# Kernel tuning notes

Measured on AMD Instinct MI355X. Metric: run time of the kernel, lower is better.

## Reference

```python
import jax, jax.numpy as jnp
import numpy as np

EMBED = 8      # == n_qubits, forced by x[:, i, :].view(batch, n_qubits)
FFN = 4096
B, S = 32, 2048


def setup_inputs() -> dict:
    key = jax.random.key(0)
    k_x, k_t, k_w1, k_b1, k_w2, k_b2 = jax.random.split(key, 6)
    x = jax.random.normal(k_x, (B, S, EMBED), dtype=jnp.float32)
    theta = jax.random.normal(k_t, (), dtype=jnp.float32)  # shared trainable RY angle
    # torch.nn.Linear-style init bounds
    lim1 = 1.0 / np.sqrt(EMBED)
    lim2 = 1.0 / np.sqrt(FFN)
    W1 = jax.random.uniform(k_w1, (FFN, EMBED), jnp.float32, -lim1, lim1)
    b1 = jax.random.uniform(k_b1, (FFN,), jnp.float32, -lim1, lim1)
    W2 = jax.random.uniform(k_w2, (EMBED, FFN), jnp.float32, -lim2, lim2)
    b2 = jax.random.uniform(k_b2, (EMBED,), jnp.float32, -lim2, lim2)
    return {"x": x, "theta": theta, "W1": W1, "b1": b1, "W2": W2, "b2": b2}


def reference(x, theta, W1, b1, W2, b2):
    # Quantum circuit, solved analytically (product state, single-qubit gates):
    # |0> --RX(x_i)--RY(theta)--> <Z_i> = cos(theta) * cos(x_i)
    # This fuses the original per-token Python loop into one elementwise op.
    q = jnp.cos(theta) * jnp.cos(x)                 # [B, S, 8]
    # dropout is identity in eval mode
    h = jax.nn.relu(jnp.einsum('bsk,fk->bsf', q, W1) + b1)   # [B, S, FFN]
    out = jnp.einsum('bsf,ef->bse', h, W2) + b2              # [B, S, 8]
    return out
```

## Files before the change

kernel.cpp:

```cpp
#include <hip/hip_runtime.h>
#include <math.h>

#define FFN_DIM 4096
#define NCHUNK  128

typedef _Float16 f16x8 __attribute__((ext_vector_type(8)));
typedef __fp16   h16x2 __attribute__((ext_vector_type(2)));
typedef float    f32x16 __attribute__((ext_vector_type(16)));
typedef float    f32x4  __attribute__((ext_vector_type(4)));

__global__ void build_frags_kernel(const float* __restrict__ w1,
                                   const float* __restrict__ b1,
                                   const float* __restrict__ w2,
                                   _Float16* __restrict__ w1f,
                                   _Float16* __restrict__ w2f) {
    int i = blockIdx.x * 256 + threadIdx.x;
    if (i < NCHUNK * 64 * 8) {
        int j    = i & 7;
        int lane = (i >> 3) & 63;
        int cc   = i >> 9;
        _Float16 v;
        if (lane < 32) v = (_Float16)w1[(cc * 32 + lane) * 8 + j];
        else           v = (j == 0) ? (_Float16)b1[cc * 32 + (lane & 31)]
                                    : (_Float16)0.0f;
        w1f[i] = v;
    }
    if (i < NCHUNK * 2 * 16 * 8) {
        int j  = i & 7;
        int ci = (i >> 3) & 15;
        int c  = (i >> 7) & 1;
        int cc = i >> 8;
        int g = ci >> 3, e = ci & 7;
        int k = 8 * g + j;
        int fl = (k & 3) + 8 * ((k >> 2) & 1) + 4 * (k >> 3);
        int f = 32 * cc + 16 * c + fl;
        w2f[i] = (_Float16)w2[e * FFN_DIM + f];
    }
}

__global__ __launch_bounds__(256, 2) void ffq_mfma_kernel(
    const float* __restrict__ x,
    const float* __restrict__ theta,
    const _Float16* __restrict__ w1f,
    const _Float16* __restrict__ w2f,
    const float* __restrict__ b2,
    float* __restrict__ out,
    int n_tok)
{
    __shared__ float part[4][4][64][4];

    const int tid  = threadIdx.x;
    const int lane = tid & 63;
    const int wave = tid >> 6;
    const int l31  = lane & 31;
    const int g    = lane >> 5;

    const int tb = blockIdx.x * 128;
    const float cth = cosf(theta[0]);

    f16x8 bq0 = {}, bq1 = {}, bq2 = {}, bq3 = {};
    if (g == 0) {
#define LOAD_BQ(BQ, TOFF)                                                  \
        {                                                                  \
            int t_ = tb + (TOFF) + l31;                                    \
            int r_ = t_ < n_tok ? t_ : (n_tok - 1);                        \
            const f32x4* xp_ = (const f32x4*)(x + (size_t)r_ * 8);         \
            f32x4 u_ = xp_[0], v_ = xp_[1];                                \
            BQ[0] = (_Float16)(cth * cosf(u_.x));                          \
            BQ[1] = (_Float16)(cth * cosf(u_.y));                          \
            BQ[2] = (_Float16)(cth * cosf(u_.z));                          \
            BQ[3] = (_Float16)(cth * cosf(u_.w));                          \
            BQ[4] = (_Float16)(cth * cosf(v_.x));                          \
            BQ[5] = (_Float16)(cth * cosf(v_.y));                          \
            BQ[6] = (_Float16)(cth * cosf(v_.z));                          \
            BQ[7] = (_Float16)(cth * cosf(v_.w));                          \
        }
        LOAD_BQ(bq0, 0)
        LOAD_BQ(bq1, 32)
        LOAD_BQ(bq2, 64)
        LOAD_BQ(bq3, 96)
#undef LOAD_BQ
    } else {
        bq0[0] = (_Float16)1.0f;
        bq1[0] = (_Float16)1.0f;
        bq2[0] = (_Float16)1.0f;
        bq3[0] = (_Float16)1.0f;
    }

    f32x16 acc0 = {}, acc1 = {}, acc2 = {}, acc3 = {};
    const f32x16 zero16 = {};

    const int ci = g * 8 + (l31 & 7);
    const _Float16* a1p = w1f + (size_t)lane * 8;
    const _Float16* a2p = w2f + (size_t)ci * 8;

    union U8 { f16x8 v; h16x2 p[4]; };
    const h16x2 hz = {(__fp16)0.0f, (__fp16)0.0f};

    const int c0 = wave * (NCHUNK / 4);
    const int c1 = c0 + (NCHUNK / 4);

    for (int cc = c0; cc < c1; ++cc) {
        f16x8 A1  = *(const f16x8*)(a1p + (size_t)cc * 512);
        f16x8 A2a = *(const f16x8*)(a2p + (size_t)cc * 256);
        f16x8 A2b = *(const f16x8*)(a2p + (size_t)cc * 256 + 128);

        f32x16 dA = __builtin_amdgcn_mfma_f32_32x32x16_f16(A1, bq0, zero16, 0, 0, 0);
        f32x16 dB = __builtin_amdgcn_mfma_f32_32x32x16_f16(A1, bq1, zero16, 0, 0, 0);
        U8 uaA, ubA, uaB, ubB;
        #pragma unroll
        for (int v = 0; v < 4; ++v) {
            uaA.p[v] = __builtin_amdgcn_cvt_pkrtz(dA[2 * v],     dA[2 * v + 1]);
            ubA.p[v] = __builtin_amdgcn_cvt_pkrtz(dA[8 + 2 * v], dA[8 + 2 * v + 1]);
            uaB.p[v] = __builtin_amdgcn_cvt_pkrtz(dB[2 * v],     dB[2 * v + 1]);
            ubB.p[v] = __builtin_amdgcn_cvt_pkrtz(dB[8 + 2 * v], dB[8 + 2 * v + 1]);
        }
        #pragma unroll
        for (int v = 0; v < 4; ++v) {
            uaA.p[v] = __builtin_elementwise_max(uaA.p[v], hz);
            ubA.p[v] = __builtin_elementwise_max(ubA.p[v], hz);
            uaB.p[v] = __builtin_elementwise_max(uaB.p[v], hz);
            ubB.p[v] = __builtin_elementwise_max(ubB.p[v], hz);
        }
        acc0 = __builtin_amdgcn_mfma_f32_32x32x16_f16(A2a, uaA.v, acc0, 0, 0, 0);
        acc0 = __builtin_amdgcn_mfma_f32_32x32x16_f16(A2b, ubA.v, acc0, 0, 0, 0);
        acc1 = __builtin_amdgcn_mfma_f32_32x32x16_f16(A2a, uaB.v, acc1, 0, 0, 0);
        acc1 = __builtin_amdgcn_mfma_f32_32x32x16_f16(A2b, ubB.v, acc1, 0, 0, 0);

        f32x16 dC = __builtin_amdgcn_mfma_f32_32x32x16_f16(A1, bq2, zero16, 0, 0, 0);
        f32x16 dD = __builtin_amdgcn_mfma_f32_32x32x16_f16(A1, bq3, zero16, 0, 0, 0);
        U8 uaC, ubC, uaD, ubD;
        #pragma unroll
        for (int v = 0; v < 4; ++v) {
            uaC.p[v] = __builtin_amdgcn_cvt_pkrtz(dC[2 * v],     dC[2 * v + 1]);
            ubC.p[v] = __builtin_amdgcn_cvt_pkrtz(dC[8 + 2 * v], dC[8 + 2 * v + 1]);
            uaD.p[v] = __builtin_amdgcn_cvt_pkrtz(dD[2 * v],     dD[2 * v + 1]);
            ubD.p[v] = __builtin_amdgcn_cvt_pkrtz(dD[8 + 2 * v], dD[8 + 2 * v + 1]);
        }
        #pragma unroll
        for (int v = 0; v < 4; ++v) {
            uaC.p[v] = __builtin_elementwise_max(uaC.p[v], hz);
            ubC.p[v] = __builtin_elementwise_max(ubC.p[v], hz);
            uaD.p[v] = __builtin_elementwise_max(uaD.p[v], hz);
            ubD.p[v] = __builtin_elementwise_max(ubD.p[v], hz);
        }
        acc2 = __builtin_amdgcn_mfma_f32_32x32x16_f16(A2a, uaC.v, acc2, 0, 0, 0);
        acc2 = __builtin_amdgcn_mfma_f32_32x32x16_f16(A2b, ubC.v, acc2, 0, 0, 0);
        acc3 = __builtin_amdgcn_mfma_f32_32x32x16_f16(A2a, uaD.v, acc3, 0, 0, 0);
        acc3 = __builtin_amdgcn_mfma_f32_32x32x16_f16(A2b, ubD.v, acc3, 0, 0, 0);
    }

    #pragma unroll
    for (int r = 0; r < 4; ++r) {
        part[wave][0][lane][r] = acc0[r];
        part[wave][1][lane][r] = acc1[r];
        part[wave][2][lane][r] = acc2[r];
        part[wave][3][lane][r] = acc3[r];
    }
    __syncthreads();

    for (int i = tid; i < 128 * 8; i += 256) {
        int t = i >> 3, e = i & 7;
        int gt = tb + t;
        if (gt < n_tok) {
            int tt = t >> 5;
            int tl = t & 31;
            int sl = (e >> 2) * 32 + tl;
            int r  = e & 3;
            float s = part[0][tt][sl][r] + part[1][tt][sl][r]
                    + part[2][tt][sl][r] + part[3][tt][sl][r] + b2[e];
            out[(size_t)gt * 8 + e] = s;
        }
    }
}

__global__ __launch_bounds__(256, 4) void ffq_valu_kernel(
    const float* __restrict__ x, const float* __restrict__ theta,
    const float* __restrict__ w1, const float* __restrict__ b1,
    const float* __restrict__ w2, const float* __restrict__ b2,
    float* __restrict__ out, int n_tok)
{
    __shared__ float part[4][64][9];
    const int tid = threadIdx.x;
    const int lane = tid & 63;
    const int wave = __builtin_amdgcn_readfirstlane(tid >> 6);
    const int tok = blockIdx.x * 64 + lane;
    const int rtok = tok < n_tok ? tok : n_tok - 1;
    const float cth = cosf(theta[0]);
    const f32x4* xv = (const f32x4*)(x + (size_t)rtok * 8);
    f32x4 x0 = xv[0], x1 = xv[1];
    float q[8];
    q[0]=cth*cosf(x0.x); q[1]=cth*cosf(x0.y); q[2]=cth*cosf(x0.z); q[3]=cth*cosf(x0.w);
    q[4]=cth*cosf(x1.x); q[5]=cth*cosf(x1.y); q[6]=cth*cosf(x1.z); q[7]=cth*cosf(x1.w);
    float acc[8];
    #pragma unroll
    for (int e = 0; e < 8; ++e) acc[e] = 0.0f;
    const int f0 = wave * (FFN_DIM / 4), f1 = f0 + (FFN_DIM / 4);
    #pragma unroll 2
    for (int f = f0; f < f1; ++f) {
        const f32x4* w1r = (const f32x4*)(w1 + (size_t)f * 8);
        f32x4 u0 = w1r[0], u1 = w1r[1];
        float h = b1[f];
        h = fmaf(u0.x,q[0],h); h = fmaf(u0.y,q[1],h); h = fmaf(u0.z,q[2],h); h = fmaf(u0.w,q[3],h);
        h = fmaf(u1.x,q[4],h); h = fmaf(u1.y,q[5],h); h = fmaf(u1.z,q[6],h); h = fmaf(u1.w,q[7],h);
        h = fmaxf(h, 0.0f);
        #pragma unroll
        for (int e = 0; e < 8; ++e) acc[e] = fmaf(h, w2[e * FFN_DIM + f], acc[e]);
    }
    #pragma unroll
    for (int e = 0; e < 8; ++e) part[wave][lane][e] = acc[e];
    __syncthreads();
    for (int i = tid; i < 64 * 8; i += 256) {
        int t = i >> 3, e = i & 7;
        int gt = blockIdx.x * 64 + t;
        if (gt < n_tok)
            out[(size_t)gt * 8 + e] = part[0][t][e] + part[1][t][e]
                                    + part[2][t][e] + part[3][t][e] + b2[e];
    }
}

extern "C" void kernel_launch(void* const* d_in, const int* in_sizes, int n_in,
                              void* d_out, int out_size, void* d_ws, size_t ws_size,
                              hipStream_t stream) {
    const float* x     = (const float*)d_in[0];
    const float* theta = (const float*)d_in[1];
    const float* w1    = (const float*)d_in[2];
    const float* b1    = (const float*)d_in[3];
    const float* w2    = (const float*)d_in[4];
    const float* b2    = (const float*)d_in[5];
    float* out = (float*)d_out;
    const int n_tok = out_size / 8;

    const size_t W1F_BYTES = (size_t)NCHUNK * 64 * 8 * sizeof(_Float16);
    const size_t W2F_BYTES = (size_t)NCHUNK * 2 * 16 * 8 * sizeof(_Float16);

    if (ws_size >= W1F_BYTES + W2F_BYTES) {
        _Float16* w1f = (_Float16*)d_ws;
        _Float16* w2f = (_Float16*)((char*)d_ws + W1F_BYTES);
        build_frags_kernel<<<(NCHUNK * 64 * 8 + 255) / 256, 256, 0, stream>>>(
            w1, b1, w2, w1f, w2f);
        int blocks = (n_tok + 127) / 128;
        ffq_mfma_kernel<<<blocks, 256, 0, stream>>>(x, theta, w1f, w2f, b2, out,
                                                    n_tok);
    } else {
        int grid = (n_tok + 63) / 64;
        ffq_valu_kernel<<<grid, 256, 0, stream>>>(x, theta, w1, b1, w2, b2, out,
                                                  n_tok);
    }
}
```

Measured before the change: 33.57 us.

## Software-pipeline first-layer MFMAs one chunk ahead of ReLU pack and second GEMM

Restructures the per-wave chunk loop into a prologue, a steady-state body and an epilogue. Each iteration now issues the next chunk's first-layer MFMAs while the current chunk's results are packed to fp16 with ReLU and fed to the second-layer MFMAs. W1 fragments are prefetched two chunks ahead and W2 fragments one chunk ahead. The goal is to hide MFMA result latency and global-load latency behind independent work, and the accumulator MFMA order is interleaved so back-to-back updates do not hit the same accumulator. The cost is more live VGPRs (four extra 16-float result sets plus the prefetched fragments), which could lower occupancy or cause spills.

```diff
diff --git a/kernel.cpp b/kernel.cpp
--- a/kernel.cpp
+++ b/kernel.cpp
@@ -100,55 +100,79 @@
     const int c0 = wave * (NCHUNK / 4);
     const int c1 = c0 + (NCHUNK / 4);
 
-    for (int cc = c0; cc < c1; ++cc) {
-        f16x8 A1  = *(const f16x8*)(a1p + (size_t)cc * 512);
-        f16x8 A2a = *(const f16x8*)(a2p + (size_t)cc * 256);
-        f16x8 A2b = *(const f16x8*)(a2p + (size_t)cc * 256 + 128);
-
-        f32x16 dA = __builtin_amdgcn_mfma_f32_32x32x16_f16(A1, bq0, zero16, 0, 0, 0);
-        f32x16 dB = __builtin_amdgcn_mfma_f32_32x32x16_f16(A1, bq1, zero16, 0, 0, 0);
+    f16x8 A1c  = *(const f16x8*)(a1p + (size_t)c0 * 512);
+    f16x8 A2ap = *(const f16x8*)(a2p + (size_t)c0 * 256);
+    f16x8 A2bp = *(const f16x8*)(a2p + (size_t)c0 * 256 + 128);
+    f16x8 A1nx = *(const f16x8*)(a1p + (size_t)(c0 + 1) * 512);
+
+    f32x16 dA = __builtin_amdgcn_mfma_f32_32x32x16_f16(A1c, bq0, zero16, 0, 0, 0);
+    f32x16 dB = __builtin_amdgcn_mfma_f32_32x32x16_f16(A1c, bq1, zero16, 0, 0, 0);
+    f32x16 dC = __builtin_amdgcn_mfma_f32_32x32x16_f16(A1c, bq2, zero16, 0, 0, 0);
+    f32x16 dD = __builtin_amdgcn_mfma_f32_32x32x16_f16(A1c, bq3, zero16, 0, 0, 0);
+    A1c = A1nx;
+
+#define PACK(U_A, U_B, D)                                                  \
+    {                                                                      \
+        _Pragma("unroll")                                                  \
+        for (int v = 0; v < 4; ++v) {                                      \
+            U_A.p[v] = __builtin_amdgcn_cvt_pkrtz((D)[2 * v], (D)[2 * v + 1]); \
+            U_B.p[v] = __builtin_amdgcn_cvt_pkrtz((D)[8 + 2 * v], (D)[8 + 2 * v + 1]); \
+        }                                                                  \
+        _Pragma("unroll")                                                  \
+        for (int v = 0; v < 4; ++v) {                                      \
+            U_A.p[v] = __builtin_elementwise_max(U_A.p[v], hz);            \
+            U_B.p[v] = __builtin_elementwise_max(U_B.p[v], hz);            \
+        }                                                                  \
+    }
+
+    for (int cc = c0 + 1; cc < c1; ++cc) {
+        int nx1 = (cc + 1 < c1) ? (cc + 1) : cc;
+        f16x8 A1f  = *(const f16x8*)(a1p + (size_t)nx1 * 512);
+        f16x8 A2an = *(const f16x8*)(a2p + (size_t)cc * 256);
+        f16x8 A2bn = *(const f16x8*)(a2p + (size_t)cc * 256 + 128);
+
+        f32x16 nA = __builtin_amdgcn_mfma_f32_32x32x16_f16(A1c, bq0, zero16, 0, 0, 0);
+        f32x16 nB = __builtin_amdgcn_mfma_f32_32x32x16_f16(A1c, bq1, zero16, 0, 0, 0);
+
         U8 uaA, ubA, uaB, ubB;
-        #pragma unroll
-        for (int v = 0; v < 4; ++v) {
-            uaA.p[v] = __builtin_amdgcn_cvt_pkrtz(dA[2 * v],     dA[2 * v + 1]);
-            ubA.p[v] = __builtin_amdgcn_cvt_pkrtz(dA[8 + 2 * v], dA[8 + 2 * v + 1]);
-            uaB.p[v] = __builtin_amdgcn_cvt_pkrtz(dB[2 * v],     dB[2 * v + 1]);
-            ubB.p[v] = __builtin_amdgcn_cvt_pkrtz(dB[8 + 2 * v], dB[8 + 2 * v + 1]);
-        }
-        #pragma unroll
-        for (int v = 0; v < 4; ++v) {
-            uaA.p[v] = __builtin_elementwise_max(uaA.p[v], hz);
-            ubA.p[v] = __builtin_elementwise_max(ubA.p[v], hz);
-            uaB.p[v] = __builtin_elementwise_max(uaB.p[v], hz);
-            ubB.p[v] = __builtin_elementwise_max(ubB.p[v], hz);
-        }
-        acc0 = __builtin_amdgcn_mfma_f32_32x32x16_f16(A2a, uaA.v, acc0, 0, 0, 0);
-        acc0 = __builtin_amdgcn_mfma_f32_32x32x16_f16(A2b, ubA.v, acc0, 0, 0, 0);
-        acc1 = __builtin_amdgcn_mfma_f32_32x32x16_f16(A2a, uaB.v, acc1, 0, 0, 0);
-        acc1 = __builtin_amdgcn_mfma_f32_32x32x16_f16(A2b, ubB.v, acc1, 0, 0, 0);
-
-        f32x16 dC = __builtin_amdgcn_mfma_f32_32x32x16_f16(A1, bq2, zero16, 0, 0, 0);
-        f32x16 dD = __builtin_amdgcn_mfma_f32_32x32x16_f16(A1, bq3, zero16, 0, 0, 0);
+        PACK(uaA, ubA, dA)
+        PACK(uaB, ubB, dB)
+        acc0 = __builtin_amdgcn_mfma_f32_32x32x16_f16(A2ap, uaA.v, acc0, 0, 0, 0);
+        acc1 = __builtin_amdgcn_mfma_f32_32x32x16_f16(A2ap, uaB.v, acc1, 0, 0, 0);
+        acc0 = __builtin_amdgcn_mfma_f32_32x32x16_f16(A2bp, ubA.v, acc0, 0, 0, 0);
+        acc1 = __builtin_amdgcn_mfma_f32_32x32x16_f16(A2bp, ubB.v, acc1, 0, 0, 0);
+
+        f32x16 nC = __builtin_amdgcn_mfma_f32_32x32x16_f16(A1c, bq2, zero16, 0, 0, 0);
+        f32x16 nD = __builtin_amdgcn_mfma_f32_32x32x16_f16(A1c, bq3, zero16, 0, 0, 0);
+
         U8 uaC, ubC, uaD, ubD;
-        #pragma unroll
-        for (int v = 0; v < 4; ++v) {
-            uaC.p[v] = __builtin_amdgcn_cvt_pkrtz(dC[2 * v],     dC[2 * v + 1]);
-            ubC.p[v] = __builtin_amdgcn_cvt_pkrtz(dC[8 + 2 * v], dC[8 + 2 * v + 1]);
-            uaD.p[v] = __builtin_amdgcn_cvt_pkrtz(dD[2 * v],     dD[2 * v + 1]);
-            ubD.p[v] = __builtin_amdgcn_cvt_pkrtz(dD[8 + 2 * v], dD[8 + 2 * v + 1]);
-        }
-        #pragma unroll
-        for (int v = 0; v < 4; ++v) {
-            uaC.p[v] = __builtin_elementwise_max(uaC.p[v], hz);
-            ubC.p[v] = __builtin_elementwise_max(ubC.p[v], hz);
-            uaD.p[v] = __builtin_elementwise_max(uaD.p[v], hz);
-            ubD.p[v] = __builtin_elementwise_max(ubD.p[v], hz);
-        }
-        acc2 = __builtin_amdgcn_mfma_f32_32x32x16_f16(A2a, uaC.v, acc2, 0, 0, 0);
-        acc2 = __builtin_amdgcn_mfma_f32_32x32x16_f16(A2b, ubC.v, acc2, 0, 0, 0);
-        acc3 = __builtin_amdgcn_mfma_f32_32x32x16_f16(A2a, uaD.v, acc3, 0, 0, 0);
-        acc3 = __builtin_amdgcn_mfma_f32_32x32x16_f16(A2b, ubD.v, acc3, 0, 0, 0);
-    }
+        PACK(uaC, ubC, dC)
+        PACK(uaD, ubD, dD)
+        acc2 = __builtin_amdgcn_mfma_f32_32x32x16_f16(A2ap, uaC.v, acc2, 0, 0, 0);
+        acc3 = __builtin_amdgcn_mfma_f32_32x32x16_f16(A2ap, uaD.v, acc3, 0, 0, 0);
+        acc2 = __builtin_amdgcn_mfma_f32_32x32x16_f16(A2bp, ubC.v, acc2, 0, 0, 0);
+        acc3 = __builtin_amdgcn_mfma_f32_32x32x16_f16(A2bp, ubD.v, acc3, 0, 0, 0);
+
+        dA = nA; dB = nB; dC = nC; dD = nD;
+        A1c = A1f; A2ap = A2an; A2bp = A2bn;
+    }
+
+    {
+        U8 uaA, ubA, uaB, ubB, uaC, ubC, uaD, ubD;
+        PACK(uaA, ubA, dA)
+        PACK(uaB, ubB, dB)
+        PACK(uaC, ubC, dC)
+        PACK(uaD, ubD, dD)
+        acc0 = __builtin_amdgcn_mfma_f32_32x32x16_f16(A2ap, uaA.v, acc0, 0, 0, 0);
+        acc1 = __builtin_amdgcn_mfma_f32_32x32x16_f16(A2ap, uaB.v, acc1, 0, 0, 0);
+        acc2 = __builtin_amdgcn_mfma_f32_32x32x16_f16(A2ap, uaC.v, acc2, 0, 0, 0);
+        acc3 = __builtin_amdgcn_mfma_f32_32x32x16_f16(A2ap, uaD.v, acc3, 0, 0, 0);
+        acc0 = __builtin_amdgcn_mfma_f32_32x32x16_f16(A2bp, ubA.v, acc0, 0, 0, 0);
+        acc1 = __builtin_amdgcn_mfma_f32_32x32x16_f16(A2bp, ubB.v, acc1, 0, 0, 0);
+        acc2 = __builtin_amdgcn_mfma_f32_32x32x16_f16(A2bp, ubC.v, acc2, 0, 0, 0);
+        acc3 = __builtin_amdgcn_mfma_f32_32x32x16_f16(A2bp, ubD.v, acc3, 0, 0, 0);
+    }
+#undef PACK
 
     #pragma unroll
     for (int r = 0; r < 4; ++r) {
```

New measurement: 34.93 us. +4.1%, slower.
